# Kernel optimization log

Hardware: AMD Instinct MI355X
Metric: run time of the kernel (lower is better)

The kernel has to match this reference:

```python
import jax, jax.numpy as jnp
import numpy as np

B, K, C, L = 16, 8, 64, 2048
OFFSET = 2.0  # self.offset in Coupling
EPS = 1e-7    # clamp for logit stability (flows' safe_log analogue)


def setup_inputs() -> dict:
    key = jax.random.key(0)
    ks = jax.random.split(key, 6)
    return {
        "x_change": jax.random.normal(ks[0], (B, C, L), jnp.float32),
        "a": jax.random.normal(ks[1], (B, C, L), jnp.float32),
        "b": jax.random.normal(ks[2], (B, C, L), jnp.float32),
        "pi": jax.random.normal(ks[3], (B, K, C, L), jnp.float32),
        "mu": jax.random.normal(ks[4], (B, K, C, L), jnp.float32),
        "s": jax.random.normal(ks[5], (B, K, C, L), jnp.float32) * 0.1,  # log-scales
        "sldj": jnp.zeros((B,), jnp.float32),
    }


def reference(x_change, a, b, pi, mu, s, sldj):
    # scale = sigmoid(a + offset) + (1 - sigmoid(offset))
    sig_off = 1.0 - jax.nn.sigmoid(jnp.float32(OFFSET))
    scale = jax.nn.sigmoid(a + OFFSET) + sig_off                      # [B,C,L]

    logpi = jax.nn.log_softmax(pi, axis=1)                            # [B,K,C,L]
    z = (x_change[:, None] - mu) * jnp.exp(-s)                        # [B,K,C,L]

    # logistic.mixture_log_cdf: logsumexp_k(log pi_k + log sigmoid(z_k))
    log_cdf = jax.scipy.special.logsumexp(logpi + jax.nn.log_sigmoid(z), axis=1)
    u = jnp.clip(jnp.exp(log_cdf), EPS, 1.0 - EPS)                    # [B,C,L]

    # logistic.inverse (forward): logit, with ldj = -log(u) - log(1-u)
    y = jnp.log(u) - jnp.log1p(-u)
    scale_ldj = -jnp.log(u) - jnp.log1p(-u)

    # logistic.mixture_log_pdf: logsumexp_k(log pi_k + z - s - 2 softplus(z))
    log_pdf = jax.scipy.special.logsumexp(
        logpi + z - s - 2.0 * jax.nn.softplus(z), axis=1)             # [B,C,L]

    sldj_out = sldj + jnp.sum(
        (log_pdf + scale_ldj + jnp.log(scale)).reshape(sldj.shape[0], -1), axis=-1)
    out = (y + b) * scale                                             # [B,C,L]
    return out, sldj_out
```

## Files before the change

kernel.cpp:

```cpp
#include <hip/hip_runtime.h>

#define BB 16
#define KK 8
#define CC 64
#define LL 2048

constexpr int CL = CC * LL;
constexpr int NELEM = BB * CL;
constexpr int NBLOCKS = NELEM / 256;

#define SIG_OFF 0.11920292202211755f
#define LOG_EPS -16.11809565095832f

__device__ __forceinline__ float frcp(float x) { return __builtin_amdgcn_rcpf(x); }

__global__ void init_sldj_kernel(const float* __restrict__ sldj_in,
                                 float* __restrict__ sldj_out) {
    int i = threadIdx.x;
    if (i < BB) sldj_out[i] = sldj_in[i];
}

__global__ __launch_bounds__(256, 8) void coupling_kernel(
    const float* __restrict__ x,
    const float* __restrict__ a,
    const float* __restrict__ bv,
    const float* __restrict__ pi,
    const float* __restrict__ mu,
    const float* __restrict__ s,
    float* __restrict__ out,
    float* __restrict__ sldj_out) {

    const int idx = blockIdx.x * 256 + threadIdx.x;
    const int b   = idx >> 17;
    const int kbase = (b << 20) + (idx & (CL - 1));

    const float xe = x[idx];
    const float ae = a[idx];
    const float be = bv[idx];

    float pv[KK], mv[KK], sv[KK];
#pragma unroll
    for (int k = 0; k < KK; ++k) {
        const int o = kbase + k * CL;
        pv[k] = pi[o];
        mv[k] = mu[o];
        sv[k] = s[o];
    }
    __builtin_amdgcn_sched_barrier(0);

    float Spi = 0.f, Nc = 0.f, N1 = 0.f, Np = 0.f;

#pragma unroll
    for (int k = 0; k < KK; ++k) {
        const float invstd = __expf(-sv[k]);
        const float z      = (xe - mv[k]) * invstd;

        const float t  = __expf(-fabsf(z));
        const float r  = frcp(1.f + t);
        const float tr = t * r;
        const float sig  = (z >= 0.f) ? r  : tr;
        const float osig = (z >= 0.f) ? tr : r;

        const float ek = __expf(pv[k]);
        Spi += ek;
        Nc  += ek * sig;
        N1  += ek * osig;
        Np  += ek * invstd * sig * osig;
    }

    const float lSpi = __logf(Spi);
    const float lu   = fmaxf(__logf(Nc) - lSpi, LOG_EPS);
    const float lomu = fmaxf(__logf(N1) - lSpi, LOG_EPS);
    const float y        = lu - lomu;
    const float ldj_term = -lu - lomu;
    const float log_pdf  = __logf(Np) - lSpi;

    const float av = ae + 2.f;
    const float t2 = __expf(-fabsf(av));
    const float r2 = frcp(1.f + t2);
    const float sc = ((av >= 0.f) ? r2 : t2 * r2) + SIG_OFF;

    out[idx] = (y + be) * sc;

    float contrib = log_pdf + ldj_term + __logf(sc);

#pragma unroll
    for (int off = 32; off > 0; off >>= 1)
        contrib += __shfl_down(contrib, off, 64);

    __shared__ float wsum[4];
    const int lane = threadIdx.x & 63;
    const int wid  = threadIdx.x >> 6;
    if (lane == 0) wsum[wid] = contrib;
    __syncthreads();
    if (threadIdx.x == 0) {
        atomicAdd(&sldj_out[b], wsum[0] + wsum[1] + wsum[2] + wsum[3]);
    }
}

extern "C" void kernel_launch(void* const* d_in, const int* in_sizes, int n_in,
                              void* d_out, int out_size, void* d_ws, size_t ws_size,
                              hipStream_t stream) {
    const float* x    = (const float*)d_in[0];
    const float* a    = (const float*)d_in[1];
    const float* bv   = (const float*)d_in[2];
    const float* pi   = (const float*)d_in[3];
    const float* mu   = (const float*)d_in[4];
    const float* s    = (const float*)d_in[5];
    const float* sldj = (const float*)d_in[6];

    float* out      = (float*)d_out;
    float* sldj_out = out + (size_t)NELEM;

    init_sldj_kernel<<<1, 64, 0, stream>>>(sldj, sldj_out);
    coupling_kernel<<<NBLOCKS, 256, 0, stream>>>(x, a, bv, pi, mu, s, out, sldj_out);
}
```

Baseline: 260.7 us.

## Stage all input streams into LDS via async global_load_lds per tile

Each block now issues direct global-to-LDS 16-byte loads for all 27 input streams of its 256-element tile, with each wave handling a subset of streams, then reads operands from LDS after a barrier. The intent is to raise memory-level parallelism with wide asynchronous loads that bypass registers, which should help a bandwidth-bound kernel. In exchange it uses about 27 KB of LDS per block, which limits occupancy, drops the occupancy hint from the launch bounds, and adds a block-wide barrier before any compute can start.

```diff
diff --git a/kernel.cpp b/kernel.cpp
--- a/kernel.cpp
+++ b/kernel.cpp
@@ -1,4 +1,5 @@
 #include <hip/hip_runtime.h>
+#include <stdint.h>
 
 #define BB 16
 #define KK 8
@@ -7,12 +8,21 @@
 
 constexpr int CL = CC * LL;
 constexpr int NELEM = BB * CL;
-constexpr int NBLOCKS = NELEM / 256;
+constexpr int TILE = 256;
+constexpr int NBLOCKS = NELEM / TILE;
+constexpr int NSTREAM = 27;
 
 #define SIG_OFF 0.11920292202211755f
 #define LOG_EPS -16.11809565095832f
 
 __device__ __forceinline__ float frcp(float x) { return __builtin_amdgcn_rcpf(x); }
+
+__device__ __forceinline__ void load_to_lds16(const float* g, float* l) {
+    __builtin_amdgcn_global_load_lds(
+        (const __attribute__((address_space(1))) void*)g,
+        (__attribute__((address_space(3))) void*)l,
+        16, 0, 0);
+}
 
 __global__ void init_sldj_kernel(const float* __restrict__ sldj_in,
                                  float* __restrict__ sldj_out) {
@@ -20,7 +30,7 @@
     if (i < BB) sldj_out[i] = sldj_in[i];
 }
 
-__global__ __launch_bounds__(256, 8) void coupling_kernel(
+__global__ __launch_bounds__(256) void coupling_kernel(
     const float* __restrict__ x,
     const float* __restrict__ a,
     const float* __restrict__ bv,
@@ -30,38 +40,52 @@
     float* __restrict__ out,
     float* __restrict__ sldj_out) {
 
-    const int idx = blockIdx.x * 256 + threadIdx.x;
-    const int b   = idx >> 17;
-    const int kbase = (b << 20) + (idx & (CL - 1));
+    __shared__ float lds[NSTREAM * TILE];
 
-    const float xe = x[idx];
-    const float ae = a[idx];
-    const float be = bv[idx];
+    const int tile = blockIdx.x;
+    const int b    = tile >> 9;
+    const int base = tile * TILE;
+    const int rem  = base & (CL - 1);
+    const int kb0  = (b << 20) + rem;
 
-    float pv[KK], mv[KK], sv[KK];
-#pragma unroll
-    for (int k = 0; k < KK; ++k) {
-        const int o = kbase + k * CL;
-        pv[k] = pi[o];
-        mv[k] = mu[o];
-        sv[k] = s[o];
+    const int lane = threadIdx.x & 63;
+    const int wv   = threadIdx.x >> 6;
+
+    for (int sidx = wv; sidx < NSTREAM; sidx += 4) {
+        const float* gp;
+        if (sidx == 0)       gp = x  + base;
+        else if (sidx == 1)  gp = a  + base;
+        else if (sidx == 2)  gp = bv + base;
+        else if (sidx < 11)  gp = pi + kb0 + (sidx - 3)  * CL;
+        else if (sidx < 19)  gp = mu + kb0 + (sidx - 11) * CL;
+        else                 gp = s  + kb0 + (sidx - 19) * CL;
+        load_to_lds16(gp + lane * 4, &lds[sidx * TILE + lane * 4]);
     }
-    __builtin_amdgcn_sched_barrier(0);
+    __syncthreads();
+
+    const int t  = threadIdx.x;
+    const float xe = lds[0 * TILE + t];
+    const float ae = lds[1 * TILE + t];
+    const float be = lds[2 * TILE + t];
 
     float Spi = 0.f, Nc = 0.f, N1 = 0.f, Np = 0.f;
 
 #pragma unroll
     for (int k = 0; k < KK; ++k) {
-        const float invstd = __expf(-sv[k]);
-        const float z      = (xe - mv[k]) * invstd;
+        const float p  = lds[(3 + k)  * TILE + t];
+        const float m  = lds[(11 + k) * TILE + t];
+        const float sk = lds[(19 + k) * TILE + t];
 
-        const float t  = __expf(-fabsf(z));
-        const float r  = frcp(1.f + t);
-        const float tr = t * r;
+        const float invstd = __expf(-sk);
+        const float z      = (xe - m) * invstd;
+
+        const float tt = __expf(-fabsf(z));
+        const float r  = frcp(1.f + tt);
+        const float tr = tt * r;
         const float sig  = (z >= 0.f) ? r  : tr;
         const float osig = (z >= 0.f) ? tr : r;
 
-        const float ek = __expf(pv[k]);
+        const float ek = __expf(p);
         Spi += ek;
         Nc  += ek * sig;
         N1  += ek * osig;
@@ -80,7 +104,7 @@
     const float r2 = frcp(1.f + t2);
     const float sc = ((av >= 0.f) ? r2 : t2 * r2) + SIG_OFF;
 
-    out[idx] = (y + be) * sc;
+    out[base + t] = (y + be) * sc;
 
     float contrib = log_pdf + ldj_term + __logf(sc);
 
@@ -89,9 +113,7 @@
         contrib += __shfl_down(contrib, off, 64);
 
     __shared__ float wsum[4];
-    const int lane = threadIdx.x & 63;
-    const int wid  = threadIdx.x >> 6;
-    if (lane == 0) wsum[wid] = contrib;
+    if (lane == 0) wsum[wv] = contrib;
     __syncthreads();
     if (threadIdx.x == 0) {
         atomicAdd(&sldj_out[b], wsum[0] + wsum[1] + wsum[2] + wsum[3]);
```

After: 265.0 us. About the same (+1.6%).
